# Kernel optimization log

Measured on AMD Instinct MI355X. Metric: run time of the kernel, lower is better.

Reference implementation:

```python
import jax, jax.numpy as jnp
import numpy as np

D = 1024
NS = 12
B = 32
S = 128
K = 512


def setup_inputs() -> dict:
    key = jax.random.key(0)
    ks = jax.random.split(key, 20)
    w = 0.02  # weight scale (xavier-ish)
    return {
        "context": jax.random.normal(ks[0], (B, S, D), jnp.float32),
        "question": jax.random.normal(ks[1], (B, 2 * D), jnp.float32),
        "knowledge": jax.random.normal(ks[2], (B, D, K), jnp.float32),
        "control_init": jax.random.normal(ks[3], (1, 1), jnp.float32),
        # position-aware linears, one per step: Linear(2d, d)
        "pa_w": jax.random.normal(ks[4], (NS, D, 2 * D), jnp.float32) * w,
        "pa_b": jnp.zeros((NS, D), jnp.float32),
        # control unit
        "cq_w": jax.random.normal(ks[5], (D, 2 * D), jnp.float32) * w,
        "cq_b": jnp.zeros((D,), jnp.float32),
        "ca_w": jax.random.normal(ks[6], (1, D), jnp.float32) * w,
        "ca_b": jnp.zeros((1,), jnp.float32),
        # read unit
        "rm_w": jax.random.normal(ks[7], (D, D), jnp.float32) * w,
        "rm_b": jnp.zeros((D,), jnp.float32),
        "ri_w": jax.random.normal(ks[8], (D, 2 * D), jnp.float32) * w,
        "ri_b": jnp.zeros((D,), jnp.float32),
        "ra_w": jax.random.normal(ks[9], (1, D), jnp.float32) * w,
        "ra_b": jnp.zeros((1,), jnp.float32),
        # write unit
        "wm_w": jax.random.normal(ks[10], (D, 2 * D), jnp.float32) * w,
        "wm_b": jnp.zeros((D,), jnp.float32),
    }


def _mac_forward(context, question, knowledge, control_init,
                 pa_w, pa_b, cq_w, cq_b, ca_w, ca_b,
                 rm_w, rm_b, ri_w, ri_b, ra_w, ra_b, wm_w, wm_b):
    b = question.shape[0]
    d = pa_w.shape[1]
    know = jnp.swapaxes(knowledge, 1, 2)  # [B, K, d]
    # all position-aware projections of the question: [n_steps, B, d]
    q_pa_all = jnp.einsum('bq,sdq->sbd', question, pa_w) + pa_b[:, None, :]
    control0 = jnp.broadcast_to(control_init, (b, d))  # randn(1,1).expand(b,d)
    memory0 = q_pa_all[0]

    def step(carry, q_pa):
        control, memory = carry
        # --- control unit ---
        cq = jnp.concatenate([control, q_pa], axis=1) @ cq_w.T + cq_b  # [B, d]
        c_att = jnp.einsum('bsd,d->bs', cq[:, None, :] * context, ca_w[0]) + ca_b[0]
        c_att = jax.nn.softmax(c_att, axis=1)
        new_control = jnp.einsum('bs,bsd->bd', c_att, context)
        # --- read unit ---
        mem_p = memory @ rm_w.T + rm_b  # [B, d]
        inter = mem_p[:, None, :] * know  # [B, K, d]
        inter = jnp.concatenate([inter, know], axis=2) @ ri_w.T + ri_b  # [B, K, d]
        r_att = jnp.einsum('bkd,d->bk', new_control[:, None, :] * inter, ra_w[0]) + ra_b[0]
        r_att = jax.nn.softmax(r_att, axis=1)
        read = jnp.einsum('bk,bkd->bd', r_att, know)
        # --- write unit ---
        new_memory = jnp.concatenate([read, memory], axis=1) @ wm_w.T + wm_b
        return (new_control, new_memory), None

    (control, memory), _ = jax.lax.scan(step, (control0, memory0), q_pa_all)
    return memory


def reference(context, question, knowledge, control_init,
              pa_w, pa_b, cq_w, cq_b, ca_w, ca_b,
              rm_w, rm_b, ri_w, ri_b, ra_w, ra_b, wm_w, wm_b):
    return _mac_forward(context, question, knowledge, control_init,
                        pa_w, pa_b, cq_w, cq_b, ca_w, ca_b,
                        rm_w, rm_b, ri_w, ri_b, ra_w, ra_b, wm_w, wm_b)
```

## Files before the change

### kernel.cpp

```cpp
#include <hip/hip_runtime.h>


#define NSTEP 12

struct GemmArgs {
  const float* X1; long x1g;
  const float* X2; long x2g;
  int c1, c2;
  const float* W; int ldw; long wg;
  const float* bias; long biasg;
  const float* addend; long addg;
  const float* xscale;
  float* out; long outg;
  int N;
};

__global__ __launch_bounds__(256) void gemm32_kernel(GemmArgs a) {
  __shared__ float xs[32 * 512];
  const int g = blockIdx.y;
  const int C = a.c1 + a.c2;
  const float* X1 = a.X1 + (long)g * a.x1g;
  const float* X2 = a.X2 ? a.X2 + (long)g * a.x2g : nullptr;
  const float* W = a.W + (long)g * a.wg;
  const int wave = threadIdx.x >> 6;
  const int lane = threadIdx.x & 63;
  const int n = blockIdx.x * 4 + wave;
  const float* wrow = W + (long)n * a.ldw;
  float acc[32];
#pragma unroll
  for (int b = 0; b < 32; b++) acc[b] = 0.f;

  for (int c0 = 0; c0 < C; c0 += 512) {
    __syncthreads();
#pragma unroll
    for (int i = 0; i < 16; i++) {
      int idx = threadIdx.x + 256 * i;
      int b = idx >> 7;
      int c4 = idx & 127;
      int c = c0 + c4 * 4;
      float4 v;
      if (c < a.c1) v = *(const float4*)(X1 + (long)b * a.c1 + c);
      else          v = *(const float4*)(X2 + (long)b * a.c2 + (c - a.c1));
      if (a.xscale) {
        float4 s = *(const float4*)(a.xscale + c);
        v.x *= s.x; v.y *= s.y; v.z *= s.z; v.w *= s.w;
      }
      *(float4*)(xs + b * 512 + c4 * 4) = v;
    }
    __syncthreads();
#pragma unroll
    for (int i = 0; i < 2; i++) {
      int c = i * 256 + lane * 4;
      float4 wv = *(const float4*)(wrow + c0 + c);
#pragma unroll
      for (int b = 0; b < 32; b++) {
        float4 xv = *(const float4*)(xs + b * 512 + c);
        acc[b] += wv.x * xv.x + wv.y * xv.y + wv.z * xv.z + wv.w * xv.w;
      }
    }
  }
  float res = 0.f;
#pragma unroll
  for (int b = 0; b < 32; b++) {
    float v = acc[b];
#pragma unroll
    for (int off = 32; off; off >>= 1) v += __shfl_xor(v, off, 64);
    if (lane == b) res = v;
  }
  if (lane < 32) {
    float o = res;
    if (a.bias) o += a.bias[(long)g * a.biasg + n];
    if (a.addend) o += a.addend[(long)g * a.addg + (long)lane * a.N + n];
    a.out[(long)g * a.outg + (long)lane * a.N + n] = o;
  }
}

__global__ __launch_bounds__(1024) void init_control_kernel(const float* ci, float* control) {
  control[blockIdx.x * 1024 + threadIdx.x] = ci[0];
}

__global__ __launch_bounds__(1024) void transpose_kernel(const float* in, float* out) {
  __shared__ float t[32][33];
  int j0 = blockIdx.x * 32;
  int d0 = blockIdx.y * 32;
  int tx = threadIdx.x, ty = threadIdx.y;
  t[ty][tx] = in[(long)(d0 + ty) * 2048 + j0 + tx];
  __syncthreads();
  out[(long)(j0 + ty) * 1024 + d0 + tx] = t[tx][ty];
}

__global__ __launch_bounds__(1024) void ctrl_att_kernel(const float* cq, const float* context,
                                                        const float* ca_w, float* control) {
  int b = blockIdx.x;
  __shared__ float u[1024];
  __shared__ float sc[128];
  int tid = threadIdx.x;
  int wave = tid >> 6, lane = tid & 63;
  u[tid] = cq[b * 1024 + tid] * ca_w[tid];
  __syncthreads();
  const float* ctx = context + (long)b * 128 * 1024;
#pragma unroll
  for (int i = 0; i < 8; i++) {
    int s = wave * 8 + i;
    float v = 0.f;
#pragma unroll
    for (int c = 0; c < 16; c++) v += u[c * 64 + lane] * ctx[(long)s * 1024 + c * 64 + lane];
#pragma unroll
    for (int off = 32; off; off >>= 1) v += __shfl_xor(v, off, 64);
    if (lane == 0) sc[s] = v;
  }
  __syncthreads();
  if (wave == 0) {
    float a0 = sc[lane], a1 = sc[lane + 64];
    float m = fmaxf(a0, a1);
#pragma unroll
    for (int off = 32; off; off >>= 1) m = fmaxf(m, __shfl_xor(m, off, 64));
    float e0 = expf(a0 - m), e1 = expf(a1 - m);
    float s2 = e0 + e1;
#pragma unroll
    for (int off = 32; off; off >>= 1) s2 += __shfl_xor(s2, off, 64);
    float inv = 1.f / s2;
    sc[lane] = e0 * inv;
    sc[lane + 64] = e1 * inv;
  }
  __syncthreads();
  float acc = 0.f;
  for (int s = 0; s < 128; s++) acc += sc[s] * ctx[(long)s * 1024 + tid];
  control[b * 1024 + tid] = acc;
}

__global__ __launch_bounds__(512) void ratt_kernel(const float* knowledge, const float* mem_p,
                                                   const float* h, float* partial) {
  int b = blockIdx.x, jc = blockIdx.y;
  int j0 = jc * 64;
  __shared__ float gl[64];
  if (threadIdx.x < 64) {
    int j = j0 + threadIdx.x;
    gl[threadIdx.x] = mem_p[b * 1024 + j] * h[b * 2048 + j] + h[b * 2048 + 1024 + j];
  }
  __syncthreads();
  int k = threadIdx.x;
  const float* kb = knowledge + ((long)b * 1024 + j0) * 512 + k;
  float acc = 0.f;
#pragma unroll 8
  for (int jj = 0; jj < 64; jj++) acc += gl[jj] * kb[(long)jj * 512];
  partial[((long)jc * 32 + b) * 512 + k] = acc;
}

__global__ __launch_bounds__(256) void read_kernel(const float* partial, const float* knowledge,
                                                   float* readv) {
  int b = blockIdx.x, dg = blockIdx.y;
  __shared__ float aw[512];
  __shared__ float red[4];
  int tid = threadIdx.x;
  int wave = tid >> 6, lane = tid & 63;
  int k0 = tid * 2;
  float r0 = 0.f, r1 = 0.f;
#pragma unroll
  for (int p = 0; p < 16; p++) {
    const float* pp = partial + ((long)p * 32 + b) * 512;
    r0 += pp[k0];
    r1 += pp[k0 + 1];
  }
  float m = fmaxf(r0, r1);
#pragma unroll
  for (int off = 32; off; off >>= 1) m = fmaxf(m, __shfl_xor(m, off, 64));
  if (lane == 0) red[wave] = m;
  __syncthreads();
  m = fmaxf(fmaxf(red[0], red[1]), fmaxf(red[2], red[3]));
  __syncthreads();
  float e0 = expf(r0 - m), e1 = expf(r1 - m);
  float s2 = e0 + e1;
#pragma unroll
  for (int off = 32; off; off >>= 1) s2 += __shfl_xor(s2, off, 64);
  if (lane == 0) red[wave] = s2;
  __syncthreads();
  s2 = red[0] + red[1] + red[2] + red[3];
  float inv = 1.f / s2;
  aw[k0] = e0 * inv;
  aw[k0 + 1] = e1 * inv;
  __syncthreads();
  int d0 = dg * 32 + wave * 8;
  float acc[8];
#pragma unroll
  for (int i = 0; i < 8; i++) acc[i] = 0.f;
  const float* kb = knowledge + ((long)b * 1024 + d0) * 512;
  for (int kc = 0; kc < 8; kc++) {
    int kk = kc * 64 + lane;
    float av = aw[kk];
#pragma unroll
    for (int dd = 0; dd < 8; dd++) acc[dd] += av * kb[(long)dd * 512 + kk];
  }
#pragma unroll
  for (int dd = 0; dd < 8; dd++) {
    float v = acc[dd];
#pragma unroll
    for (int off = 32; off; off >>= 1) v += __shfl_xor(v, off, 64);
    if (lane == dd) readv[b * 1024 + d0 + dd] = v;
  }
}

static inline void launch_gemm(const float* X1, long x1g, const float* X2, long x2g,
                               int c1, int c2, const float* W, int ldw, long wg,
                               const float* bias, long biasg,
                               const float* addend, long addg,
                               const float* xscale, float* out, long outg, int N, int G,
                               hipStream_t stream) {
  GemmArgs a{X1, x1g, X2, x2g, c1, c2, W, ldw, wg, bias, biasg, addend, addg, xscale, out, outg, N};
  gemm32_kernel<<<dim3(N / 4, G), 256, 0, stream>>>(a);
}

extern "C" void kernel_launch(void* const* d_in, const int* in_sizes, int n_in,
                              void* d_out, int out_size, void* d_ws, size_t ws_size,
                              hipStream_t stream) {
  const float* context      = (const float*)d_in[0];
  const float* question     = (const float*)d_in[1];
  const float* knowledge    = (const float*)d_in[2];
  const float* control_init = (const float*)d_in[3];
  const float* pa_w = (const float*)d_in[4];
  const float* pa_b = (const float*)d_in[5];
  const float* cq_w = (const float*)d_in[6];
  const float* cq_b = (const float*)d_in[7];
  const float* ca_w = (const float*)d_in[8];
  const float* rm_w = (const float*)d_in[10];
  const float* rm_b = (const float*)d_in[11];
  const float* ri_w = (const float*)d_in[12];
  const float* ra_w = (const float*)d_in[14];
  const float* wm_w = (const float*)d_in[16];
  const float* wm_b = (const float*)d_in[17];
  float* out = (float*)d_out;

  float* p = (float*)d_ws;
  float* q_pa_all = p; p += NSTEP * 32 * 1024;
  float* qc_all   = p; p += NSTEP * 32 * 1024;
  float* ri_wT    = p; p += 2048 * 1024;
  float* control  = p; p += 32 * 1024;
  float* mem0     = p; p += 32 * 1024;
  float* mem1     = p; p += 32 * 1024;
  float* cq       = p; p += 32 * 1024;
  float* mem_p    = p; p += 32 * 1024;
  float* h        = p; p += 32 * 2048;
  float* partial  = p; p += 16 * 32 * 512;
  float* readv    = p; p += 32 * 1024;

  init_control_kernel<<<32, 1024, 0, stream>>>(control_init, control);
  transpose_kernel<<<dim3(64, 32), dim3(32, 32), 0, stream>>>(ri_w, ri_wT);
  launch_gemm(question, 0, nullptr, 0, 2048, 0, pa_w, 2048, 1024L * 2048,
              pa_b, 1024, nullptr, 0, nullptr, q_pa_all, 32 * 1024, 1024, NSTEP, stream);
  hipMemcpyAsync(mem0, q_pa_all, 32 * 1024 * sizeof(float), hipMemcpyDeviceToDevice, stream);
  launch_gemm(q_pa_all, 32 * 1024, nullptr, 0, 1024, 0, cq_w + 1024, 2048, 0,
              nullptr, 0, nullptr, 0, nullptr, qc_all, 32 * 1024, 1024, NSTEP, stream);

  float* mems[2] = {mem0, mem1};
  for (int s = 0; s < NSTEP; s++) {
    float* mo = mems[s & 1];
    float* mn = (s == NSTEP - 1) ? out : mems[(s + 1) & 1];
    launch_gemm(control, 0, nullptr, 0, 1024, 0, cq_w, 2048, 0,
                cq_b, 0, qc_all + (long)s * 32 * 1024, 0, nullptr, cq, 0, 1024, 1, stream);
    launch_gemm(mo, 0, nullptr, 0, 1024, 0, rm_w, 1024, 0,
                rm_b, 0, nullptr, 0, nullptr, mem_p, 0, 1024, 1, stream);
    ctrl_att_kernel<<<32, 1024, 0, stream>>>(cq, context, ca_w, control);
    launch_gemm(control, 0, nullptr, 0, 1024, 0, ri_wT, 1024, 0,
                nullptr, 0, nullptr, 0, ra_w, h, 0, 2048, 1, stream);
    ratt_kernel<<<dim3(32, 16), 512, 0, stream>>>(knowledge, mem_p, h, partial);
    read_kernel<<<dim3(32, 32), 256, 0, stream>>>(partial, knowledge, readv);
    launch_gemm(readv, 0, mo, 0, 1024, 1024, wm_w, 2048, 0,
                wm_b, 0, nullptr, 0, nullptr, mn, 0, 1024, 1, stream);
  }
}
```

Before: 1.671 ms.

## Switch GEMMs to transposed activation layout with split-K batched jobs

Replaces the shared-memory GEMM with a kernel that stores activations as [C,32] and weights transposed as [C,N]. Each lane owns one output column, eight waves split the K dimension, and partials are reduced through shared memory. Independent GEMMs (cq and rm projections, and split-K halves) run together in one launch through a job array, with partial sums folded into consumer kernels. ra_w is pre-multiplied into ri_w once. The aim is fewer launches and more parallel blocks for the tiny batch-32 GEMMs, at the cost of extra transposes and workspace.

```diff
diff --git a/kernel.cpp b/kernel.cpp
--- a/kernel.cpp
+++ b/kernel.cpp
@@ -3,100 +3,104 @@
 
 #define NSTEP 12
 
-struct GemmArgs {
-  const float* X1; long x1g;
-  const float* X2; long x2g;
-  int c1, c2;
-  const float* W; int ldw; long wg;
-  const float* bias; long biasg;
-  const float* addend; long addg;
-  const float* xscale;
-  float* out; long outg;
-  int N;
+struct GJob {
+  const float* X1;
+  const float* X2;
+  const float* Wt;
+  const float* bias;
+  float* out;
+  long xg, wg, bg, og;
+  int c1, N, cbeg, clen, rm;
 };
 
-__global__ __launch_bounds__(256) void gemm32_kernel(GemmArgs a) {
-  __shared__ float xs[32 * 512];
+struct GArgs4 { GJob j[4]; };
+
+__global__ __launch_bounds__(512) void gemm_xt(GArgs4 A) {
+  __shared__ float red[7 * 64 * 32];
+  const GJob j = A.j[blockIdx.z];
+  const int lane = threadIdx.x & 63;
+  const int wave = threadIdx.x >> 6;
   const int g = blockIdx.y;
-  const int C = a.c1 + a.c2;
-  const float* X1 = a.X1 + (long)g * a.x1g;
-  const float* X2 = a.X2 ? a.X2 + (long)g * a.x2g : nullptr;
-  const float* W = a.W + (long)g * a.wg;
-  const int wave = threadIdx.x >> 6;
-  const int lane = threadIdx.x & 63;
-  const int n = blockIdx.x * 4 + wave;
-  const float* wrow = W + (long)n * a.ldw;
+  const int n = blockIdx.x * 64 + lane;
+  const int CW = j.clen >> 3;
+  const int cb = j.cbeg + wave * CW;
+  const float* __restrict__ xt =
+      (cb < j.c1) ? j.X1 + (long)g * j.xg + (long)cb * 32
+                  : j.X2 + (long)(cb - j.c1) * 32;
+  const float* __restrict__ wt = j.Wt + (long)g * j.wg + (long)cb * j.N + n;
   float acc[32];
 #pragma unroll
   for (int b = 0; b < 32; b++) acc[b] = 0.f;
-
-  for (int c0 = 0; c0 < C; c0 += 512) {
-    __syncthreads();
-#pragma unroll
-    for (int i = 0; i < 16; i++) {
-      int idx = threadIdx.x + 256 * i;
-      int b = idx >> 7;
-      int c4 = idx & 127;
-      int c = c0 + c4 * 4;
-      float4 v;
-      if (c < a.c1) v = *(const float4*)(X1 + (long)b * a.c1 + c);
-      else          v = *(const float4*)(X2 + (long)b * a.c2 + (c - a.c1));
-      if (a.xscale) {
-        float4 s = *(const float4*)(a.xscale + c);
-        v.x *= s.x; v.y *= s.y; v.z *= s.z; v.w *= s.w;
+  for (int c = 0; c < CW; ++c) {
+    float w = wt[(long)c * j.N];
+    const float* __restrict__ xr = xt + c * 32;
+#pragma unroll
+    for (int b = 0; b < 32; b++) acc[b] = fmaf(xr[b], w, acc[b]);
+  }
+  if (wave) {
+    float* r = red + (wave - 1) * 64 * 32 + lane * 32;
+#pragma unroll
+    for (int b = 0; b < 32; b += 4)
+      *(float4*)(r + b) = make_float4(acc[b], acc[b + 1], acc[b + 2], acc[b + 3]);
+  }
+  __syncthreads();
+  if (wave == 0) {
+#pragma unroll
+    for (int w = 0; w < 7; w++) {
+      const float* r = red + w * 64 * 32 + lane * 32;
+#pragma unroll
+      for (int b = 0; b < 32; b += 4) {
+        float4 v = *(const float4*)(r + b);
+        acc[b] += v.x; acc[b + 1] += v.y; acc[b + 2] += v.z; acc[b + 3] += v.w;
       }
-      *(float4*)(xs + b * 512 + c4 * 4) = v;
-    }
-    __syncthreads();
-#pragma unroll
-    for (int i = 0; i < 2; i++) {
-      int c = i * 256 + lane * 4;
-      float4 wv = *(const float4*)(wrow + c0 + c);
-#pragma unroll
-      for (int b = 0; b < 32; b++) {
-        float4 xv = *(const float4*)(xs + b * 512 + c);
-        acc[b] += wv.x * xv.x + wv.y * xv.y + wv.z * xv.z + wv.w * xv.w;
-      }
-    }
-  }
-  float res = 0.f;
-#pragma unroll
-  for (int b = 0; b < 32; b++) {
-    float v = acc[b];
-#pragma unroll
-    for (int off = 32; off; off >>= 1) v += __shfl_xor(v, off, 64);
-    if (lane == b) res = v;
-  }
-  if (lane < 32) {
-    float o = res;
-    if (a.bias) o += a.bias[(long)g * a.biasg + n];
-    if (a.addend) o += a.addend[(long)g * a.addg + (long)lane * a.N + n];
-    a.out[(long)g * a.outg + (long)lane * a.N + n] = o;
-  }
-}
-
-__global__ __launch_bounds__(1024) void init_control_kernel(const float* ci, float* control) {
-  control[blockIdx.x * 1024 + threadIdx.x] = ci[0];
-}
-
-__global__ __launch_bounds__(1024) void transpose_kernel(const float* in, float* out) {
+    }
+    float bv = j.bias ? j.bias[(long)g * j.bg + n] : 0.f;
+    if (j.rm) {
+      float* o = j.out + (long)g * j.og + n;
+#pragma unroll
+      for (int b = 0; b < 32; b++) o[(long)b * j.N] = acc[b] + bv;
+    } else {
+      float* o = j.out + (long)g * j.og + (long)n * 32;
+#pragma unroll
+      for (int b = 0; b < 32; b += 4)
+        *(float4*)(o + b) = make_float4(acc[b] + bv, acc[b + 1] + bv,
+                                        acc[b + 2] + bv, acc[b + 3] + bv);
+    }
+  }
+}
+
+__global__ __launch_bounds__(1024) void transpose_k(const float* in, float* out,
+                                                    int R, int C, long ing, long outg) {
   __shared__ float t[32][33];
-  int j0 = blockIdx.x * 32;
-  int d0 = blockIdx.y * 32;
-  int tx = threadIdx.x, ty = threadIdx.y;
-  t[ty][tx] = in[(long)(d0 + ty) * 2048 + j0 + tx];
-  __syncthreads();
-  out[(long)(j0 + ty) * 1024 + d0 + tx] = t[tx][ty];
-}
-
-__global__ __launch_bounds__(1024) void ctrl_att_kernel(const float* cq, const float* context,
-                                                        const float* ca_w, float* control) {
+  const float* I = in + (long)blockIdx.z * ing;
+  float* O = out + (long)blockIdx.z * outg;
+  int c0 = blockIdx.x * 32, r0 = blockIdx.y * 32;
+  t[threadIdx.y][threadIdx.x] = I[(long)(r0 + threadIdx.y) * C + c0 + threadIdx.x];
+  __syncthreads();
+  O[(long)(c0 + threadIdx.y) * R + r0 + threadIdx.x] = t[threadIdx.x][threadIdx.y];
+}
+
+__global__ __launch_bounds__(1024) void init_control_kernel(const float* ci, float* control_t) {
+  control_t[blockIdx.x * 1024 + threadIdx.x] = ci[0];
+}
+
+__global__ __launch_bounds__(1024) void riws_kernel(const float* ri_w, const float* ra_w,
+                                                    float* riws) {
+  int i = blockIdx.x * 1024 + threadIdx.x;
+  riws[i] = ri_w[i] * ra_w[i >> 11];
+}
+
+__global__ __launch_bounds__(1024) void ctrl_att_kernel(const float* cq_p, const float* qc_s,
+                                                        const float* cq_b, const float* context,
+                                                        const float* ca_w, float* control_t) {
   int b = blockIdx.x;
   __shared__ float u[1024];
   __shared__ float sc[128];
   int tid = threadIdx.x;
   int wave = tid >> 6, lane = tid & 63;
-  u[tid] = cq[b * 1024 + tid] * ca_w[tid];
+  float cqv = cq_p[tid * 32 + b] + cq_p[32 * 1024 + tid * 32 + b] +
+              qc_s[tid * 32 + b] + cq_b[tid];
+  u[tid] = cqv * ca_w[tid];
   __syncthreads();
   const float* ctx = context + (long)b * 128 * 1024;
 #pragma unroll
@@ -126,17 +130,21 @@
   __syncthreads();
   float acc = 0.f;
   for (int s = 0; s < 128; s++) acc += sc[s] * ctx[(long)s * 1024 + tid];
-  control[b * 1024 + tid] = acc;
-}
-
-__global__ __launch_bounds__(512) void ratt_kernel(const float* knowledge, const float* mem_p,
-                                                   const float* h, float* partial) {
+  control_t[tid * 32 + b] = acc;
+}
+
+__global__ __launch_bounds__(512) void ratt_kernel(const float* knowledge, const float* memp_p,
+                                                   const float* h_p, const float* rm_b,
+                                                   float* partial) {
   int b = blockIdx.x, jc = blockIdx.y;
   int j0 = jc * 64;
   __shared__ float gl[64];
   if (threadIdx.x < 64) {
     int j = j0 + threadIdx.x;
-    gl[threadIdx.x] = mem_p[b * 1024 + j] * h[b * 2048 + j] + h[b * 2048 + 1024 + j];
+    float mp = memp_p[j * 32 + b] + memp_p[32 * 1024 + j * 32 + b] + rm_b[j];
+    float h1 = h_p[j * 32 + b] + h_p[2048 * 32 + j * 32 + b];
+    float h2 = h_p[(1024 + j) * 32 + b] + h_p[2048 * 32 + (1024 + j) * 32 + b];
+    gl[threadIdx.x] = mp * h1 + h2;
   }
   __syncthreads();
   int k = threadIdx.x;
@@ -148,7 +156,7 @@
 }
 
 __global__ __launch_bounds__(256) void read_kernel(const float* partial, const float* knowledge,
-                                                   float* readv) {
+                                                   float* read_t) {
   int b = blockIdx.x, dg = blockIdx.y;
   __shared__ float aw[512];
   __shared__ float red[4];
@@ -196,18 +204,17 @@
     float v = acc[dd];
 #pragma unroll
     for (int off = 32; off; off >>= 1) v += __shfl_xor(v, off, 64);
-    if (lane == dd) readv[b * 1024 + d0 + dd] = v;
-  }
-}
-
-static inline void launch_gemm(const float* X1, long x1g, const float* X2, long x2g,
-                               int c1, int c2, const float* W, int ldw, long wg,
-                               const float* bias, long biasg,
-                               const float* addend, long addg,
-                               const float* xscale, float* out, long outg, int N, int G,
-                               hipStream_t stream) {
-  GemmArgs a{X1, x1g, X2, x2g, c1, c2, W, ldw, wg, bias, biasg, addend, addg, xscale, out, outg, N};
-  gemm32_kernel<<<dim3(N / 4, G), 256, 0, stream>>>(a);
+    if (lane == dd) read_t[(d0 + dd) * 32 + b] = v;
+  }
+}
+
+static inline GJob mkjob(const float* X1, const float* X2, int c1, const float* Wt,
+                         const float* bias, float* out, long xg, long wg, long bg, long og,
+                         int N, int cbeg, int clen, int rm) {
+  GJob j; j.X1 = X1; j.X2 = X2; j.Wt = Wt; j.bias = bias; j.out = out;
+  j.xg = xg; j.wg = wg; j.bg = bg; j.og = og;
+  j.c1 = c1; j.N = N; j.cbeg = cbeg; j.clen = clen; j.rm = rm;
+  return j;
 }
 
 extern "C" void kernel_launch(void* const* d_in, const int* in_sizes, int n_in,
@@ -231,40 +238,89 @@
   float* out = (float*)d_out;
 
   float* p = (float*)d_ws;
-  float* q_pa_all = p; p += NSTEP * 32 * 1024;
-  float* qc_all   = p; p += NSTEP * 32 * 1024;
-  float* ri_wT    = p; p += 2048 * 1024;
-  float* control  = p; p += 32 * 1024;
-  float* mem0     = p; p += 32 * 1024;
-  float* mem1     = p; p += 32 * 1024;
-  float* cq       = p; p += 32 * 1024;
-  float* mem_p    = p; p += 32 * 1024;
-  float* h        = p; p += 32 * 2048;
-  float* partial  = p; p += 16 * 32 * 512;
-  float* readv    = p; p += 32 * 1024;
-
-  init_control_kernel<<<32, 1024, 0, stream>>>(control_init, control);
-  transpose_kernel<<<dim3(64, 32), dim3(32, 32), 0, stream>>>(ri_w, ri_wT);
-  launch_gemm(question, 0, nullptr, 0, 2048, 0, pa_w, 2048, 1024L * 2048,
-              pa_b, 1024, nullptr, 0, nullptr, q_pa_all, 32 * 1024, 1024, NSTEP, stream);
-  hipMemcpyAsync(mem0, q_pa_all, 32 * 1024 * sizeof(float), hipMemcpyDeviceToDevice, stream);
-  launch_gemm(q_pa_all, 32 * 1024, nullptr, 0, 1024, 0, cq_w + 1024, 2048, 0,
-              nullptr, 0, nullptr, 0, nullptr, qc_all, 32 * 1024, 1024, NSTEP, stream);
-
-  float* mems[2] = {mem0, mem1};
+  float* cqT       = p; p += 2048 * 1024;
+  float* rmT       = p; p += 1024 * 1024;
+  float* wmT       = p; p += 2048 * 1024;
+  float* riws      = p; p += 1024 * 2048;
+  float* questionT = p; p += 2048 * 32;
+  float* q_pa_t    = p; p += NSTEP * 1024 * 32;
+  float* qc_t      = p; p += NSTEP * 1024 * 32;
+  float* control_t = p; p += 1024 * 32;
+  float* memA      = p; p += 1024 * 32;
+  float* memB      = p; p += 1024 * 32;
+  float* cq_p      = p; p += 2 * 1024 * 32;
+  float* memp_p    = p; p += 2 * 1024 * 32;
+  float* h_p       = p; p += 2 * 2048 * 32;
+  float* partial   = p; p += 16 * 32 * 512;
+  float* read_t    = p; p += 1024 * 32;
+  float* paT       = p;
+
+  long used = (long)(p - (float*)d_ws);
+  long avail = (long)(ws_size / 4) - used;
+  int GC = (int)(avail / (2048L * 1024));
+  if (GC > NSTEP) GC = NSTEP;
+  if (GC < 1) GC = 1;
+
+  transpose_k<<<dim3(64, 32, 1), dim3(32, 32), 0, stream>>>(cq_w, cqT, 1024, 2048, 0, 0);
+  transpose_k<<<dim3(32, 32, 1), dim3(32, 32), 0, stream>>>(rm_w, rmT, 1024, 1024, 0, 0);
+  transpose_k<<<dim3(64, 32, 1), dim3(32, 32), 0, stream>>>(wm_w, wmT, 1024, 2048, 0, 0);
+  transpose_k<<<dim3(64, 1, 1), dim3(32, 32), 0, stream>>>(question, questionT, 32, 2048, 0, 0);
+  riws_kernel<<<2048, 1024, 0, stream>>>(ri_w, ra_w, riws);
+  init_control_kernel<<<32, 1024, 0, stream>>>(control_init, control_t);
+
+  for (int s0 = 0; s0 < NSTEP; s0 += GC) {
+    int gc = NSTEP - s0 < GC ? NSTEP - s0 : GC;
+    transpose_k<<<dim3(64, 32, gc), dim3(32, 32), 0, stream>>>(
+        pa_w + (long)s0 * 1024 * 2048, paT, 1024, 2048, 2048L * 1024, 2048L * 1024);
+    GArgs4 A;
+    A.j[0] = mkjob(questionT, nullptr, 1 << 30, paT, pa_b + (long)s0 * 1024,
+                   q_pa_t + (long)s0 * 1024 * 32, 0, 2048L * 1024, 1024, 1024 * 32,
+                   1024, 0, 2048, 0);
+    A.j[1] = A.j[0]; A.j[2] = A.j[0]; A.j[3] = A.j[0];
+    gemm_xt<<<dim3(16, gc, 1), 512, 0, stream>>>(A);
+  }
+  {
+    GArgs4 A;
+    A.j[0] = mkjob(q_pa_t, nullptr, 1 << 30, cqT + 1024 * 1024, nullptr, qc_t,
+                   1024 * 32, 0, 0, 1024 * 32, 1024, 0, 1024, 0);
+    A.j[1] = A.j[0]; A.j[2] = A.j[0]; A.j[3] = A.j[0];
+    gemm_xt<<<dim3(16, NSTEP, 1), 512, 0, stream>>>(A);
+  }
+
   for (int s = 0; s < NSTEP; s++) {
-    float* mo = mems[s & 1];
-    float* mn = (s == NSTEP - 1) ? out : mems[(s + 1) & 1];
-    launch_gemm(control, 0, nullptr, 0, 1024, 0, cq_w, 2048, 0,
-                cq_b, 0, qc_all + (long)s * 32 * 1024, 0, nullptr, cq, 0, 1024, 1, stream);
-    launch_gemm(mo, 0, nullptr, 0, 1024, 0, rm_w, 1024, 0,
-                rm_b, 0, nullptr, 0, nullptr, mem_p, 0, 1024, 1, stream);
-    ctrl_att_kernel<<<32, 1024, 0, stream>>>(cq, context, ca_w, control);
-    launch_gemm(control, 0, nullptr, 0, 1024, 0, ri_wT, 1024, 0,
-                nullptr, 0, nullptr, 0, ra_w, h, 0, 2048, 1, stream);
-    ratt_kernel<<<dim3(32, 16), 512, 0, stream>>>(knowledge, mem_p, h, partial);
-    read_kernel<<<dim3(32, 32), 256, 0, stream>>>(partial, knowledge, readv);
-    launch_gemm(readv, 0, mo, 0, 1024, 1024, wm_w, 2048, 0,
-                wm_b, 0, nullptr, 0, nullptr, mn, 0, 1024, 1, stream);
-  }
-}
+    const float* mo = (s == 0) ? q_pa_t : ((s & 1) ? memA : memB);
+    float* mn = (s == NSTEP - 1) ? out : ((s & 1) ? memB : memA);
+    {
+      GArgs4 A;
+      A.j[0] = mkjob(control_t, nullptr, 1 << 30, cqT, nullptr, cq_p,
+                     0, 0, 0, 0, 1024, 0, 512, 0);
+      A.j[1] = mkjob(control_t, nullptr, 1 << 30, cqT, nullptr, cq_p + 1024 * 32,
+                     0, 0, 0, 0, 1024, 512, 512, 0);
+      A.j[2] = mkjob(mo, nullptr, 1 << 30, rmT, nullptr, memp_p,
+                     0, 0, 0, 0, 1024, 0, 512, 0);
+      A.j[3] = mkjob(mo, nullptr, 1 << 30, rmT, nullptr, memp_p + 1024 * 32,
+                     0, 0, 0, 0, 1024, 512, 512, 0);
+      gemm_xt<<<dim3(16, 1, 4), 512, 0, stream>>>(A);
+    }
+    ctrl_att_kernel<<<32, 1024, 0, stream>>>(cq_p, qc_t + (long)s * 1024 * 32, cq_b,
+                                             context, ca_w, control_t);
+    {
+      GArgs4 A;
+      A.j[0] = mkjob(control_t, nullptr, 1 << 30, riws, nullptr, h_p,
+                     0, 0, 0, 0, 2048, 0, 512, 0);
+      A.j[1] = mkjob(control_t, nullptr, 1 << 30, riws, nullptr, h_p + 2048 * 32,
+                     0, 0, 0, 0, 2048, 512, 512, 0);
+      A.j[2] = A.j[0]; A.j[3] = A.j[0];
+      gemm_xt<<<dim3(32, 1, 2), 512, 0, stream>>>(A);
+    }
+    ratt_kernel<<<dim3(32, 16), 512, 0, stream>>>(knowledge, memp_p, h_p, rm_b, partial);
+    read_kernel<<<dim3(32, 32), 256, 0, stream>>>(partial, knowledge, read_t);
+    {
+      GArgs4 A;
+      A.j[0] = mkjob(read_t, mo, 1024, wmT, wm_b, mn,
+                     0, 0, 0, 0, 1024, 0, 2048, (s == NSTEP - 1) ? 1 : 0);
+      A.j[1] = A.j[0]; A.j[2] = A.j[0]; A.j[3] = A.j[0];
+      gemm_xt<<<dim3(16, 1, 1), 512, 0, stream>>>(A);
+    }
+  }
+}
```

Measured after the change: 3.191 ms. +91.0%, slower.

## Batch step GEMMs, compute multiple outputs per wave, fold ra_w into weights

Applied to the files above, without the earlier changes.

The GEMM kernel is rewritten so each wave computes U output columns, reusing each shared-memory X load across U weight rows, and the K-chunk is halved to 256. The cq and mem_p GEMMs of each step are merged into a single launch using blockIdx.z as a job selector. The ra_w scaling moves from a per-step xscale multiply into the one-time transposed ri_w weights, and the memcpy of the initial memory is replaced by reading q_pa directly. The trade-off is more registers per thread and fewer blocks per launch for the per-step GEMMs.

```diff
diff --git a/kernel.cpp b/kernel.cpp
--- a/kernel.cpp
+++ b/kernel.cpp
@@ -3,75 +3,79 @@
 
 #define NSTEP 12
 
-struct GemmArgs {
-  const float* X1; long x1g;
-  const float* X2; long x2g;
-  int c1, c2;
-  const float* W; int ldw; long wg;
-  const float* bias; long biasg;
-  const float* addend; long addg;
-  const float* xscale;
-  float* out; long outg;
-  int N;
+struct GJob {
+  const float* X1;
+  const float* X2;
+  const float* W;
+  const float* bias;
+  const float* add;
+  float* out;
+  long xg, wg, bg, og;
+  int c1, C, ldw, N;
 };
-
-__global__ __launch_bounds__(256) void gemm32_kernel(GemmArgs a) {
-  __shared__ float xs[32 * 512];
+struct GJobs { GJob j[2]; };
+
+template <int U>
+__global__ __launch_bounds__(256) void gemm_k(GJobs A) {
+  __shared__ float xs[32 * 256];
+  const GJob j = A.j[blockIdx.z];
+  const int lane = threadIdx.x & 63;
+  const int wave = threadIdx.x >> 6;
   const int g = blockIdx.y;
-  const int C = a.c1 + a.c2;
-  const float* X1 = a.X1 + (long)g * a.x1g;
-  const float* X2 = a.X2 ? a.X2 + (long)g * a.x2g : nullptr;
-  const float* W = a.W + (long)g * a.wg;
-  const int wave = threadIdx.x >> 6;
-  const int lane = threadIdx.x & 63;
-  const int n = blockIdx.x * 4 + wave;
-  const float* wrow = W + (long)n * a.ldw;
-  float acc[32];
-#pragma unroll
-  for (int b = 0; b < 32; b++) acc[b] = 0.f;
-
-  for (int c0 = 0; c0 < C; c0 += 512) {
+  const int n0 = blockIdx.x * (4 * U) + wave * U;
+  const float* __restrict__ X1 = j.X1 + (long)g * j.xg;
+  const float* __restrict__ Wp = j.W + (long)g * j.wg;
+  const int C = j.C, c1 = j.c1;
+  const int cs2 = C - c1;
+  float acc[U][32];
+#pragma unroll
+  for (int u = 0; u < U; u++)
+#pragma unroll
+    for (int b = 0; b < 32; b++) acc[u][b] = 0.f;
+
+  for (int c0 = 0; c0 < C; c0 += 256) {
     __syncthreads();
 #pragma unroll
-    for (int i = 0; i < 16; i++) {
-      int idx = threadIdx.x + 256 * i;
-      int b = idx >> 7;
-      int c4 = idx & 127;
+    for (int i = 0; i < 8; i++) {
+      int idx = threadIdx.x + i * 256;
+      int b = idx >> 6, c4 = idx & 63;
       int c = c0 + c4 * 4;
       float4 v;
-      if (c < a.c1) v = *(const float4*)(X1 + (long)b * a.c1 + c);
-      else          v = *(const float4*)(X2 + (long)b * a.c2 + (c - a.c1));
-      if (a.xscale) {
-        float4 s = *(const float4*)(a.xscale + c);
-        v.x *= s.x; v.y *= s.y; v.z *= s.z; v.w *= s.w;
-      }
-      *(float4*)(xs + b * 512 + c4 * 4) = v;
+      if (c < c1) v = *(const float4*)(X1 + (long)b * c1 + c);
+      else        v = *(const float4*)(j.X2 + (long)b * cs2 + (c - c1));
+      *(float4*)(xs + b * 256 + c4 * 4) = v;
     }
     __syncthreads();
-#pragma unroll
-    for (int i = 0; i < 2; i++) {
-      int c = i * 256 + lane * 4;
-      float4 wv = *(const float4*)(wrow + c0 + c);
-#pragma unroll
-      for (int b = 0; b < 32; b++) {
-        float4 xv = *(const float4*)(xs + b * 512 + c);
-        acc[b] += wv.x * xv.x + wv.y * xv.y + wv.z * xv.z + wv.w * xv.w;
-      }
-    }
-  }
-  float res = 0.f;
-#pragma unroll
-  for (int b = 0; b < 32; b++) {
-    float v = acc[b];
-#pragma unroll
-    for (int off = 32; off; off >>= 1) v += __shfl_xor(v, off, 64);
-    if (lane == b) res = v;
-  }
-  if (lane < 32) {
-    float o = res;
-    if (a.bias) o += a.bias[(long)g * a.biasg + n];
-    if (a.addend) o += a.addend[(long)g * a.addg + (long)lane * a.N + n];
-    a.out[(long)g * a.outg + (long)lane * a.N + n] = o;
+    const int cl = lane * 4;
+    float4 wv[U];
+#pragma unroll
+    for (int u = 0; u < U; u++)
+      wv[u] = *(const float4*)(Wp + (long)(n0 + u) * j.ldw + c0 + cl);
+#pragma unroll
+    for (int b = 0; b < 32; b++) {
+      float4 xv = *(const float4*)(xs + b * 256 + cl);
+#pragma unroll
+      for (int u = 0; u < U; u++)
+        acc[u][b] += xv.x * wv[u].x + xv.y * wv[u].y + xv.z * wv[u].z + xv.w * wv[u].w;
+    }
+  }
+#pragma unroll
+  for (int u = 0; u < U; u++) {
+    float res = 0.f;
+#pragma unroll
+    for (int b = 0; b < 32; b++) {
+      float v = acc[u][b];
+#pragma unroll
+      for (int off = 32; off; off >>= 1) v += __shfl_xor(v, off, 64);
+      if (lane == b) res = v;
+    }
+    if (lane < 32) {
+      const int n = n0 + u;
+      float o = res;
+      if (j.bias) o += j.bias[(long)g * j.bg + n];
+      if (j.add) o += j.add[(long)lane * j.N + n];
+      j.out[(long)g * j.og + (long)lane * j.N + n] = o;
+    }
   }
 }
 
@@ -79,14 +83,13 @@
   control[blockIdx.x * 1024 + threadIdx.x] = ci[0];
 }
 
-__global__ __launch_bounds__(1024) void transpose_kernel(const float* in, float* out) {
+__global__ void riwsT_kernel(const float* ri_w, const float* ra_w, float* o) {
   __shared__ float t[32][33];
-  int j0 = blockIdx.x * 32;
-  int d0 = blockIdx.y * 32;
-  int tx = threadIdx.x, ty = threadIdx.y;
-  t[ty][tx] = in[(long)(d0 + ty) * 2048 + j0 + tx];
-  __syncthreads();
-  out[(long)(j0 + ty) * 1024 + d0 + tx] = t[tx][ty];
+  int j0 = blockIdx.x * 32, d0 = blockIdx.y * 32;
+  t[threadIdx.y][threadIdx.x] =
+      ri_w[(long)(d0 + threadIdx.y) * 2048 + j0 + threadIdx.x] * ra_w[d0 + threadIdx.y];
+  __syncthreads();
+  o[(long)(j0 + threadIdx.y) * 1024 + d0 + threadIdx.x] = t[threadIdx.x][threadIdx.y];
 }
 
 __global__ __launch_bounds__(1024) void ctrl_att_kernel(const float* cq, const float* context,
@@ -200,14 +203,13 @@
   }
 }
 
-static inline void launch_gemm(const float* X1, long x1g, const float* X2, long x2g,
-                               int c1, int c2, const float* W, int ldw, long wg,
-                               const float* bias, long biasg,
-                               const float* addend, long addg,
-                               const float* xscale, float* out, long outg, int N, int G,
-                               hipStream_t stream) {
-  GemmArgs a{X1, x1g, X2, x2g, c1, c2, W, ldw, wg, bias, biasg, addend, addg, xscale, out, outg, N};
-  gemm32_kernel<<<dim3(N / 4, G), 256, 0, stream>>>(a);
+static inline GJob mkjob(const float* X1, const float* X2, int c1, int C,
+                         const float* W, int ldw, const float* bias, const float* add,
+                         float* out, int N, long xg, long wg, long bg, long og) {
+  GJob j; j.X1 = X1; j.X2 = X2; j.W = W; j.bias = bias; j.add = add; j.out = out;
+  j.xg = xg; j.wg = wg; j.bg = bg; j.og = og;
+  j.c1 = c1; j.C = C; j.ldw = ldw; j.N = N;
+  return j;
 }
 
 extern "C" void kernel_launch(void* const* d_in, const int* in_sizes, int n_in,
@@ -231,40 +233,62 @@
   float* out = (float*)d_out;
 
   float* p = (float*)d_ws;
-  float* q_pa_all = p; p += NSTEP * 32 * 1024;
-  float* qc_all   = p; p += NSTEP * 32 * 1024;
-  float* ri_wT    = p; p += 2048 * 1024;
-  float* control  = p; p += 32 * 1024;
-  float* mem0     = p; p += 32 * 1024;
-  float* mem1     = p; p += 32 * 1024;
-  float* cq       = p; p += 32 * 1024;
-  float* mem_p    = p; p += 32 * 1024;
-  float* h        = p; p += 32 * 2048;
-  float* partial  = p; p += 16 * 32 * 512;
-  float* readv    = p; p += 32 * 1024;
-
+  float* riwsT   = p; p += 2048 * 1024;
+  float* q_pa    = p; p += NSTEP * 32 * 1024;
+  float* qc      = p; p += NSTEP * 32 * 1024;
+  float* control = p; p += 32 * 1024;
+  float* memA    = p; p += 32 * 1024;
+  float* memB    = p; p += 32 * 1024;
+  float* cq      = p; p += 32 * 1024;
+  float* mem_p   = p; p += 32 * 1024;
+  float* h       = p; p += 32 * 2048;
+  float* partial = p; p += 16 * 32 * 512;
+  float* readv   = p; p += 32 * 1024;
+
+  riwsT_kernel<<<dim3(64, 32), dim3(32, 32), 0, stream>>>(ri_w, ra_w, riwsT);
   init_control_kernel<<<32, 1024, 0, stream>>>(control_init, control);
-  transpose_kernel<<<dim3(64, 32), dim3(32, 32), 0, stream>>>(ri_w, ri_wT);
-  launch_gemm(question, 0, nullptr, 0, 2048, 0, pa_w, 2048, 1024L * 2048,
-              pa_b, 1024, nullptr, 0, nullptr, q_pa_all, 32 * 1024, 1024, NSTEP, stream);
-  hipMemcpyAsync(mem0, q_pa_all, 32 * 1024 * sizeof(float), hipMemcpyDeviceToDevice, stream);
-  launch_gemm(q_pa_all, 32 * 1024, nullptr, 0, 1024, 0, cq_w + 1024, 2048, 0,
-              nullptr, 0, nullptr, 0, nullptr, qc_all, 32 * 1024, 1024, NSTEP, stream);
-
-  float* mems[2] = {mem0, mem1};
+  {
+    GJobs A;
+    A.j[0] = mkjob(question, nullptr, 2048, 2048, pa_w, 2048, pa_b, nullptr,
+                   q_pa, 1024, 0, 1024L * 2048, 1024, 32 * 1024);
+    A.j[1] = A.j[0];
+    gemm_k<4><<<dim3(64, NSTEP, 1), 256, 0, stream>>>(A);
+  }
+  {
+    GJobs A;
+    A.j[0] = mkjob(q_pa, nullptr, 1024, 1024, cq_w + 1024, 2048, nullptr, nullptr,
+                   qc, 1024, 32 * 1024, 0, 0, 32 * 1024);
+    A.j[1] = A.j[0];
+    gemm_k<4><<<dim3(64, NSTEP, 1), 256, 0, stream>>>(A);
+  }
+
   for (int s = 0; s < NSTEP; s++) {
-    float* mo = mems[s & 1];
-    float* mn = (s == NSTEP - 1) ? out : mems[(s + 1) & 1];
-    launch_gemm(control, 0, nullptr, 0, 1024, 0, cq_w, 2048, 0,
-                cq_b, 0, qc_all + (long)s * 32 * 1024, 0, nullptr, cq, 0, 1024, 1, stream);
-    launch_gemm(mo, 0, nullptr, 0, 1024, 0, rm_w, 1024, 0,
-                rm_b, 0, nullptr, 0, nullptr, mem_p, 0, 1024, 1, stream);
+    const float* mo = (s == 0) ? q_pa : ((s & 1) ? memA : memB);
+    float* mn = (s == NSTEP - 1) ? out : ((s & 1) ? memB : memA);
+    {
+      GJobs A;
+      A.j[0] = mkjob(control, nullptr, 1024, 1024, cq_w, 2048, cq_b,
+                     qc + (long)s * 32 * 1024, cq, 1024, 0, 0, 0, 0);
+      A.j[1] = mkjob(mo, nullptr, 1024, 1024, rm_w, 1024, rm_b, nullptr,
+                     mem_p, 1024, 0, 0, 0, 0);
+      gemm_k<2><<<dim3(128, 1, 2), 256, 0, stream>>>(A);
+    }
     ctrl_att_kernel<<<32, 1024, 0, stream>>>(cq, context, ca_w, control);
-    launch_gemm(control, 0, nullptr, 0, 1024, 0, ri_wT, 1024, 0,
-                nullptr, 0, nullptr, 0, ra_w, h, 0, 2048, 1, stream);
+    {
+      GJobs A;
+      A.j[0] = mkjob(control, nullptr, 1024, 1024, riwsT, 1024, nullptr, nullptr,
+                     h, 2048, 0, 0, 0, 0);
+      A.j[1] = A.j[0];
+      gemm_k<2><<<dim3(256, 1, 1), 256, 0, stream>>>(A);
+    }
     ratt_kernel<<<dim3(32, 16), 512, 0, stream>>>(knowledge, mem_p, h, partial);
     read_kernel<<<dim3(32, 32), 256, 0, stream>>>(partial, knowledge, readv);
-    launch_gemm(readv, 0, mo, 0, 1024, 1024, wm_w, 2048, 0,
-                wm_b, 0, nullptr, 0, nullptr, mn, 0, 1024, 1, stream);
-  }
-}
+    {
+      GJobs A;
+      A.j[0] = mkjob(readv, mo, 1024, 2048, wm_w, 2048, wm_b, nullptr,
+                     mn, 1024, 0, 0, 0, 0);
+      A.j[1] = A.j[0];
+      gemm_k<2><<<dim3(128, 1, 1), 256, 0, stream>>>(A);
+    }
+  }
+}
```

New measurement: 1.871 ms. +12.0%, slower.
